# Optimization experiments

Hardware: AMD Instinct MI355X
Metric: run time of the kernel (lower is better)

The kernel has to match this reference:

```python
import jax, jax.numpy as jnp
import numpy as np

B, S, D, H, DH, FF = 4, 4096, 1024, 16, 64, 2048
EPS = 1e-6


def setup_inputs() -> dict:
    key = jax.random.key(0)
    ks = jax.random.split(key, 8)
    s = 0.02
    return {
        "x": jax.random.normal(ks[0], (B, S, D), jnp.float32),
        "scale": jnp.ones((D,), jnp.float32),
        "qw": jax.random.normal(ks[1], (DH * H, D), jnp.float32) * s,
        "qb": jnp.zeros((DH * H,), jnp.float32),
        "kw": jax.random.normal(ks[2], (DH * H, D), jnp.float32) * s,
        "kb": jnp.zeros((DH * H,), jnp.float32),
        "vw": jax.random.normal(ks[3], (DH * H, D), jnp.float32) * s,
        "vb": jnp.zeros((DH * H,), jnp.float32),
        "ow": jax.random.normal(ks[4], (D, DH * H), jnp.float32) * s,
        "ob": jnp.zeros((D,), jnp.float32),
        "f1w": jax.random.normal(ks[5], (FF, D), jnp.float32) * s,
        "f1b": jnp.zeros((FF,), jnp.float32),
        "f2w": jax.random.normal(ks[6], (D, FF), jnp.float32) * s,
        "f2b": jnp.zeros((D,), jnp.float32),
    }


def reference(x, scale, qw, qb, kw, kb, vw, vb, ow, ob, f1w, f1b, f2w, f2b):
    def rms(h):
        return h / jnp.sqrt(jnp.mean(h * h, axis=-1, keepdims=True) + EPS) * scale

    # --- attention (faithful to the module's unusual permutes) ---
    xn = rms(x)
    q = (xn @ qw.T + qb).reshape(B, S, DH, H).transpose(0, 3, 2, 1)  # [B,H,DH,S]
    k = (xn @ kw.T + kb).reshape(B, S, DH, H).transpose(0, 3, 1, 2)  # [B,H,S,DH]
    v = (xn @ vw.T + vb).reshape(B, S, DH, H).transpose(0, 3, 2, 1)  # [B,H,DH,S]
    # scores contract over the SEQUENCE axis -> [B,H,DH,DH]
    att = jax.nn.softmax(jnp.einsum('bhds,bhse->bhde', q, k) / jnp.sqrt(jnp.float32(DH)), axis=-1)
    a = jnp.einsum('bhde,bhes->bhds', att, v)  # [B,H,DH,S]
    # torch: permute(0,2,1,3).reshape(B,-1,DH*H); row-major split of (DH,H,S) -> (S, DH*H)
    a = a.transpose(0, 2, 1, 3).reshape(B, S, DH * H)
    x = a @ ow.T + ob + x

    # --- FFN with the repo's 'SwiGLU' = x*sigmoid(x) + x ---
    xn = rms(x)
    h = xn @ f1w.T + f1b
    h = h * jax.nn.sigmoid(h) + h
    x = h @ f2w.T + f2b + x
    return x
```

## Files before the change

### kernel.cpp

```cpp
#include <hip/hip_runtime.h>
#include <math.h>

typedef unsigned short u16;
typedef __attribute__((ext_vector_type(4))) unsigned short us4;
typedef __attribute__((ext_vector_type(8))) unsigned short us8;
typedef __attribute__((ext_vector_type(4))) float f4;
typedef __attribute__((ext_vector_type(8))) short bf16x8;
typedef __attribute__((ext_vector_type(4))) float f32x4;

#define S_LEN   4096
#define D_MODEL 1024
#define N_HEAD  16
#define D_HEAD  64
#define FF_DIM  2048
#define TOKENS  16384

__device__ __forceinline__ float bf2f(u16 u) {
  union { float f; unsigned u; } x; x.u = ((unsigned)u) << 16; return x.f;
}
__device__ __forceinline__ u16 f2bf(float f) {
  union { float f; unsigned u; } x; x.f = f;
  return (u16)((x.u + 0x7FFFu + ((x.u >> 16) & 1u)) >> 16);
}

__device__ __forceinline__ void gll16(const void* g, void* l) {
  __builtin_amdgcn_global_load_lds(
      (const __attribute__((address_space(1))) void*)g,
      (__attribute__((address_space(3))) void*)l, 16, 0, 0);
}

#define BARF() do { __builtin_amdgcn_s_barrier(); asm volatile("" ::: "memory"); } while (0)

__global__ void __launch_bounds__(256)
cvt6_k(const float* __restrict__ qw, const float* __restrict__ kw,
       const float* __restrict__ vw, const float* __restrict__ ow,
       const float* __restrict__ f1w, const float* __restrict__ f2w,
       u16* __restrict__ wq, u16* __restrict__ wk, u16* __restrict__ wv,
       u16* __restrict__ wo, u16* __restrict__ w1, u16* __restrict__ w2)
{
  const int id = blockIdx.x;
  const float* src; u16* dst; int base;
  if      (id < 1024) { src = qw;  dst = wq; base = 0; }
  else if (id < 2048) { src = kw;  dst = wk; base = 1024; }
  else if (id < 3072) { src = vw;  dst = wv; base = 2048; }
  else if (id < 4096) { src = ow;  dst = wo; base = 3072; }
  else if (id < 6144) { src = f1w; dst = w1; base = 4096; }
  else                { src = f2w; dst = w2; base = 6144; }
  const size_t i = ((size_t)(id - base) * 256 + threadIdx.x) * 4;
  const f4 v = *(const f4*)(src + i);
  us4 o;
  o[0] = f2bf(v[0]); o[1] = f2bf(v[1]); o[2] = f2bf(v[2]); o[3] = f2bf(v[3]);
  *(us4*)(dst + i) = o;
}

__global__ void __launch_bounds__(256)
rmsnorm_k(const float* __restrict__ in, const float* __restrict__ scale,
          u16* __restrict__ out)
{
  const int row = blockIdx.x;
  const int tid = threadIdx.x;
  const f4 v = *(const f4*)(in + (size_t)row * D_MODEL + tid * 4);
  float ss = v[0]*v[0] + v[1]*v[1] + v[2]*v[2] + v[3]*v[3];
#pragma unroll
  for (int off = 32; off > 0; off >>= 1) ss += __shfl_down(ss, off, 64);
  __shared__ float red[4];
  const int wid = tid >> 6, lane = tid & 63;
  if (lane == 0) red[wid] = ss;
  __syncthreads();
  const float tot = red[0] + red[1] + red[2] + red[3];
  const float r = rsqrtf(tot * (1.0f / 1024.0f) + 1e-6f);
  const f4 sc = *(const f4*)(scale + tid * 4);
  us4 o;
  o[0] = f2bf(v[0] * r * sc[0]);
  o[1] = f2bf(v[1] * r * sc[1]);
  o[2] = f2bf(v[2] * r * sc[2]);
  o[3] = f2bf(v[3] * r * sc[3]);
  *(us4*)(out + (size_t)row * D_MODEL + tid * 4) = o;
}

template<int EPI>
__global__ __launch_bounds__(512, 2)
void g8k(const u16* __restrict__ Ag, const u16* __restrict__ Wg,
         const float* __restrict__ bq, const float* __restrict__ bk,
         const float* __restrict__ bv, const float* __restrict__ res,
         void* __restrict__ C0, void* __restrict__ C1, void* __restrict__ C2,
         int N, int K)
{
  __shared__ __align__(16) u16 lds[65536];
  const int tid = threadIdx.x;
  const int w = tid >> 6, l = tid & 63;
  const int fr = l & 15, fq = l >> 4;
  const int wm = w >> 2, wn = w & 3;
  const int m0 = blockIdx.x << 8, n0 = blockIdx.y << 8;
  const int srow = w * 8 + (l >> 3);
  const int scol = ((l & 7) ^ (l >> 3)) << 3;
  const int NT = K >> 6;

  auto STAGE = [&](int isA, int hf, int bfs, int nt) {
    const u16* G = isA ? Ag : Wg;
    const int rb = (isA ? m0 : n0) + hf * 128 + srow;
    const int ks = (nt < NT ? nt << 6 : 0) + scol;
    u16* lb = lds + (isA ? 0 : 32768) + bfs * 16384 + hf * 8192 + w * 512;
    gll16(G + (size_t)rb * K + ks, lb);
    gll16(G + (size_t)(rb + 64) * K + ks, lb + 4096);
  };

  f32x4 acc[8][4] = {};
  bf16x8 afr[4][2], bfr[2][2];

  auto LDA = [&](int bf, int mh) {
#pragma unroll
    for (int i = 0; i < 4; ++i)
#pragma unroll
      for (int kk = 0; kk < 2; ++kk)
        afr[i][kk] = *(const bf16x8*)(lds + bf * 16384 + mh * 8192
                                      + (i * 32 + wm * 16 + fr) * 64
                                      + ((kk * 32 + fq * 8) ^ ((fr & 7) << 3)));
  };
  auto LDB = [&](int bf, int nh) {
#pragma unroll
    for (int jn = 0; jn < 2; ++jn)
#pragma unroll
      for (int kk = 0; kk < 2; ++kk)
        bfr[jn][kk] = *(const bf16x8*)(lds + 32768 + bf * 16384 + nh * 8192
                                       + (jn * 64 + wn * 16 + fr) * 64
                                       + ((kk * 32 + fq * 8) ^ ((fr & 7) << 3)));
  };
  auto MM = [&](int mhalf, int nhalf) {
    __builtin_amdgcn_s_setprio(1);
#pragma unroll
    for (int i = 0; i < 4; ++i)
#pragma unroll
      for (int jn = 0; jn < 2; ++jn)
#pragma unroll
        for (int kk = 0; kk < 2; ++kk)
          acc[mhalf * 4 + i][nhalf * 2 + jn] =
              __builtin_amdgcn_mfma_f32_16x16x32_bf16(afr[i][kk], bfr[jn][kk],
                                                      acc[mhalf * 4 + i][nhalf * 2 + jn], 0, 0, 0);
    __builtin_amdgcn_s_setprio(0);
  };

  STAGE(1, 0, 0, 0);
  STAGE(0, 0, 0, 0);
  STAGE(0, 1, 0, 0);
  STAGE(1, 1, 0, 0);
  STAGE(1, 0, 1, 1);
  STAGE(1, 1, 1, 1);
  asm volatile("s_waitcnt vmcnt(4)" ::: "memory");
  BARF();

  const int NIT = K >> 7;
  for (int it = 0; it < NIT; ++it) {
#pragma unroll
    for (int hf2 = 0; hf2 < 2; ++hf2) {
      const int n = 2 * it + hf2;
      const int bf = n & 1;
      LDA(bf, 0); LDB(bf, 0);
      STAGE(0, 0, bf ^ 1, n + 1);
      BARF();
      MM(0, 0);
      BARF();
      LDB(bf, 1);
      STAGE(0, 1, bf ^ 1, n + 1);
      BARF();
      MM(0, 1);
      BARF();
      LDA(bf, 1);
      STAGE(1, 0, bf, n + 2);
      BARF();
      MM(1, 1);
      BARF();
      LDB(bf, 0);
      STAGE(1, 1, bf, n + 2);
      BARF();
      MM(1, 0);
      asm volatile("s_waitcnt vmcnt(4)" ::: "memory");
      BARF();
    }
  }
  asm volatile("s_waitcnt vmcnt(0)" ::: "memory");
  __builtin_amdgcn_s_barrier();
  asm volatile("" ::: "memory");

  if constexpr (EPI == 2) {
    float* C = (float*)C0;
#pragma unroll
    for (int mi = 0; mi < 8; ++mi)
#pragma unroll
      for (int ni = 0; ni < 4; ++ni) {
        const int c = n0 + ni * 64 + wn * 16 + fr;
        const int r0 = m0 + mi * 32 + wm * 16 + fq * 4;
        const float bb = bq[c];
#pragma unroll
        for (int j = 0; j < 4; ++j)
          C[(size_t)(r0 + j) * N + c] = acc[mi][ni][j] + bb + res[(size_t)(r0 + j) * N + c];
      }
  } else if constexpr (EPI == 3) {
    u16* C = (u16*)C0;
#pragma unroll
    for (int mi = 0; mi < 8; ++mi)
#pragma unroll
      for (int ni = 0; ni < 4; ++ni) {
        const int c = n0 + ni * 64 + wn * 16 + fr;
        const int r0 = m0 + mi * 32 + wm * 16 + fq * 4;
        const float bb = bq[c];
#pragma unroll
        for (int j = 0; j < 4; ++j) {
          const float v = acc[mi][ni][j] + bb;
          const float sig = 1.0f / (1.0f + expf(-v));
          C[(size_t)(r0 + j) * N + c] = f2bf(v * sig + v);
        }
      }
  } else {
    const int z = blockIdx.y >> 2;
    const float* bias = z == 0 ? bq : (z == 1 ? bk : bv);
    const int n0l = n0 & 1023;
    const int bb = m0 >> 12, s0l = m0 & (S_LEN - 1);
#pragma unroll
    for (int mi = 0; mi < 8; ++mi)
#pragma unroll
      for (int ni = 0; ni < 4; ++ni) {
        const int c = ni * 64 + wn * 16 + fr;
        const int r0 = mi * 32 + wm * 16 + fq * 4;
        const float bv_ = bias[n0l + c];
        us4 pk;
#pragma unroll
        for (int j = 0; j < 4; ++j) pk[j] = f2bf(acc[mi][ni][j] + bv_);
        const int byte = ((c << 9) + (r0 << 1)) ^ ((c & 7) << 4);
        *(us4*)((char*)lds + byte) = pk;
      }
    __syncthreads();
    if (z < 2) {
      u16* Cout = z == 0 ? (u16*)C0 : (u16*)C1;
      const int c = tid & 255, half = tid >> 8;
      const int o = n0l + c, d = o >> 4, h = o & 15;
      const int xr = (c & 7) << 4;
      u16* dst = Cout + ((size_t)((bb << 10) + (h << 6) + d)) * S_LEN + s0l + half * 128;
#pragma unroll
      for (int u = 0; u < 16; ++u) {
        const int byte = ((c << 9) + (half << 8) + (u << 4)) ^ xr;
        const us8 v = *(const us8*)((char*)lds + byte);
        *(us8*)(dst + u * 8) = v;
      }
    } else {
      u16* Cv = (u16*)C2;
      const int d0 = n0l >> 4;
#pragma unroll
      for (int q2 = 0; q2 < 8; ++q2) {
        const int idx = q2 * 512 + tid;
        const int h = idx >> 8, r = idx & 255;
        const int xr = (h & 7) << 4;
        us8 lo, hi;
#pragma unroll
        for (int dl = 0; dl < 8; ++dl) {
          lo[dl] = *(const u16*)((char*)lds + ((((h + dl * 16) << 9) + (r << 1)) ^ xr));
          hi[dl] = *(const u16*)((char*)lds + ((((h + (dl + 8) * 16) << 9) + (r << 1)) ^ xr));
        }
        u16* dst = Cv + ((size_t)(bb * 16 + h) * S_LEN + s0l + r) * 64 + d0;
        *(us8*)dst = lo;
        *(us8*)(dst + 8) = hi;
      }
    }
  }
}

__global__ void __launch_bounds__(256)
att_sm_k(const u16* __restrict__ qt, const u16* __restrict__ kt,
         u16* __restrict__ P)
{
  __shared__ float red[4][64][64];
  const int bh = blockIdx.x;
  const int tid = threadIdx.x, w = tid >> 6, l = tid & 63;
  const int fr = l & 15, fq = l >> 4;
  const u16* Qb = qt + (size_t)bh * D_HEAD * S_LEN;
  const u16* Kb = kt + (size_t)bh * D_HEAD * S_LEN;
  f32x4 acc[4][4] = {};
  const int sb = w * 1024 + fq * 8;
  for (int ks = 0; ks < 32; ++ks) {
    const int s0 = sb + ks * 32;
    bf16x8 a[4], b[4];
#pragma unroll
    for (int m = 0; m < 4; ++m)
      a[m] = *(const bf16x8*)(Qb + (size_t)(m*16 + fr) * S_LEN + s0);
#pragma unroll
    for (int n = 0; n < 4; ++n)
      b[n] = *(const bf16x8*)(Kb + (size_t)(n*16 + fr) * S_LEN + s0);
#pragma unroll
    for (int m = 0; m < 4; ++m)
#pragma unroll
      for (int n = 0; n < 4; ++n)
        acc[m][n] = __builtin_amdgcn_mfma_f32_16x16x32_bf16(a[m], b[n], acc[m][n], 0, 0, 0);
  }
#pragma unroll
  for (int m = 0; m < 4; ++m)
#pragma unroll
    for (int n = 0; n < 4; ++n)
      *(f32x4*)&red[w][n*16 + fr][m*16 + fq*4] = acc[m][n];
  __syncthreads();

  const int d = tid >> 2, sub = tid & 3;
  float p[16];
  float mx = -1e30f;
#pragma unroll
  for (int i = 0; i < 16; ++i) {
    const int e = sub * 16 + i;
    float v = red[0][e][d] + red[1][e][d] + red[2][e][d] + red[3][e][d];
    v *= 0.125f;
    p[i] = v; mx = fmaxf(mx, v);
  }
  mx = fmaxf(mx, __shfl_xor(mx, 1, 64));
  mx = fmaxf(mx, __shfl_xor(mx, 2, 64));
  float sm = 0.0f;
#pragma unroll
  for (int i = 0; i < 16; ++i) { p[i] = expf(p[i] - mx); sm += p[i]; }
  sm += __shfl_xor(sm, 1, 64);
  sm += __shfl_xor(sm, 2, 64);
  const float inv = 1.0f / sm;
  us8 o0, o1;
#pragma unroll
  for (int i = 0; i < 8; ++i) { o0[i] = f2bf(p[i] * inv); o1[i] = f2bf(p[i+8] * inv); }
  u16* dst = P + (size_t)bh * 4096 + d * 64 + sub * 16;
  *(us8*)dst = o0;
  *(us8*)(dst + 8) = o1;
}

__global__ void __launch_bounds__(256)
pv2_k(const u16* __restrict__ P, const u16* __restrict__ v2,
      u16* __restrict__ ar)
{
  const int bh = blockIdx.x, sc = blockIdx.y;
  const int b = bh >> 4, h = bh & 15;
  const int tid = threadIdx.x, w = tid >> 6, l = tid & 63;
  const int fr = l & 15, fq = l >> 4;
  const u16* Pb = P + (size_t)bh * 4096;
  const u16* Vb = v2 + (size_t)bh * D_HEAD * S_LEN;

  bf16x8 a[4][2];
#pragma unroll
  for (int m = 0; m < 4; ++m)
#pragma unroll
    for (int ks = 0; ks < 2; ++ks)
      a[m][ks] = *(const bf16x8*)(Pb + (m*16 + fr) * 64 + ks*32 + fq*8);

  const int sw = sc * 512 + w * 128;
  f32x4 acc[8][4] = {};
#pragma unroll
  for (int n = 0; n < 8; ++n) {
    const u16* vp = Vb + (size_t)(sw + n*16 + fr) * 64 + fq*8;
    const bf16x8 b0 = *(const bf16x8*)(vp);
    const bf16x8 b1 = *(const bf16x8*)(vp + 32);
#pragma unroll
    for (int m = 0; m < 4; ++m)
      acc[n][m] = __builtin_amdgcn_mfma_f32_16x16x32_bf16(a[m][0], b0, acc[n][m], 0, 0, 0);
#pragma unroll
    for (int m = 0; m < 4; ++m)
      acc[n][m] = __builtin_amdgcn_mfma_f32_16x16x32_bf16(a[m][1], b1, acc[n][m], 0, 0, 0);
  }

  const int shi = sc >> 1;
  const int col0 = (sc & 1) * 512 + w * 128;
#pragma unroll
  for (int m = 0; m < 4; ++m)
#pragma unroll
    for (int j = 0; j < 4; ++j) {
      const int d = m*16 + fq*4 + j;
      const size_t base = ((size_t)b * 4096 + (d << 6) + (h << 2) + shi) * 1024 + col0;
#pragma unroll
      for (int n = 0; n < 8; ++n)
        ar[base + n*16 + fr] = f2bf(acc[n][m][j]);
    }
}

extern "C" void kernel_launch(void* const* d_in, const int* in_sizes, int n_in,
                              void* d_out, int out_size, void* d_ws, size_t ws_size,
                              hipStream_t stream)
{
  const float* x     = (const float*)d_in[0];
  const float* scale = (const float*)d_in[1];
  const float* qw = (const float*)d_in[2];
  const float* qb = (const float*)d_in[3];
  const float* kw = (const float*)d_in[4];
  const float* kb = (const float*)d_in[5];
  const float* vw = (const float*)d_in[6];
  const float* vb = (const float*)d_in[7];
  const float* ow = (const float*)d_in[8];
  const float* ob = (const float*)d_in[9];
  const float* f1w = (const float*)d_in[10];
  const float* f1b = (const float*)d_in[11];
  const float* f2w = (const float*)d_in[12];
  const float* f2b = (const float*)d_in[13];
  float* out = (float*)d_out;

  const size_t TOKD = (size_t)TOKENS * D_MODEL;
  const size_t WSZ1 = (size_t)D_MODEL * D_MODEL;
  const size_t WSZ2 = (size_t)FF_DIM * D_MODEL;
  u16* xn = (u16*)d_ws;
  u16* qt = xn + TOKD;
  u16* kt = qt + TOKD;
  u16* v2 = kt + TOKD;
  u16* wq = v2 + TOKD;
  u16* wk = wq + WSZ1;
  u16* wv = wk + WSZ1;
  u16* wo = wv + WSZ1;
  u16* w1 = wo + WSZ1;
  u16* w2 = w1 + WSZ2;
  u16* Patt = w2 + WSZ2;
  u16* hbuf = kt;
  u16* ar = qt;

  dim3 blk(256);
  dim3 blk8(512);

  cvt6_k<<<8192, blk, 0, stream>>>(qw, kw, vw, ow, f1w, f2w, wq, wk, wv, wo, w1, w2);
  rmsnorm_k<<<TOKENS, blk, 0, stream>>>(x, scale, xn);
  g8k<0><<<dim3(TOKENS / 256, 12), blk8, 0, stream>>>(
      xn, wq, qb, kb, vb, nullptr, qt, kt, v2, 3072, D_MODEL);
  att_sm_k<<<64, blk, 0, stream>>>(qt, kt, Patt);
  pv2_k<<<dim3(64, 8), blk, 0, stream>>>(Patt, v2, ar);
  g8k<2><<<dim3(TOKENS / 256, D_MODEL / 256), blk8, 0, stream>>>(
      ar, wo, ob, nullptr, nullptr, x, out, nullptr, nullptr, D_MODEL, D_MODEL);
  rmsnorm_k<<<TOKENS, blk, 0, stream>>>(out, scale, xn);
  g8k<3><<<dim3(TOKENS / 256, FF_DIM / 256), blk8, 0, stream>>>(
      xn, w1, f1b, nullptr, nullptr, nullptr, hbuf, nullptr, nullptr, FF_DIM, D_MODEL);
  g8k<2><<<dim3(TOKENS / 256, D_MODEL / 256), blk8, 0, stream>>>(
      hbuf, w2, f2b, nullptr, nullptr, out, out, nullptr, nullptr, D_MODEL, FF_DIM);
}
```

Before: 432.9 us.

## Restructure GEMM main loop: load all B fragments once, stream A per chunk

Replaces the 8-phase ping-pong GEMM loop, which had many barriers per K-tile, with a simpler double-buffered loop. B fragments for all four N-subtiles are loaded once per K-tile, and A fragments are loaded per 16-row chunk just before their MFMAs. This cuts barriers to two per K-tile and changes the prefetch order so that A and B for the next tile go into the alternate buffer. It raises register pressure for B fragments and may expose LDS latency more, since A loads now sit directly in front of their MFMAs.

Result: slower. 442.1 us (+2.1%).

```diff
diff --git a/kernel.cpp b/kernel.cpp
--- a/kernel.cpp
+++ b/kernel.cpp
@@ -106,77 +106,54 @@
   };
 
   f32x4 acc[8][4] = {};
-  bf16x8 afr[4][2], bfr[2][2];
-
-  auto LDA = [&](int bf, int mh) {
-#pragma unroll
-    for (int i = 0; i < 4; ++i)
+  bf16x8 b_frag[4][2];
+
+  auto LDB_ALL = [&](int bf) {
+#pragma unroll
+    for (int ni = 0; ni < 4; ++ni)
 #pragma unroll
       for (int kk = 0; kk < 2; ++kk)
-        afr[i][kk] = *(const bf16x8*)(lds + bf * 16384 + mh * 8192
-                                      + (i * 32 + wm * 16 + fr) * 64
-                                      + ((kk * 32 + fq * 8) ^ ((fr & 7) << 3)));
+        b_frag[ni][kk] = *(const bf16x8*)(lds + 32768 + bf * 16384 + (ni >> 1) * 8192
+                                          + ((ni & 1) * 64 + wn * 16 + fr) * 64
+                                          + ((kk * 32 + fq * 8) ^ ((fr & 7) << 3)));
   };
-  auto LDB = [&](int bf, int nh) {
-#pragma unroll
-    for (int jn = 0; jn < 2; ++jn)
-#pragma unroll
-      for (int kk = 0; kk < 2; ++kk)
-        bfr[jn][kk] = *(const bf16x8*)(lds + 32768 + bf * 16384 + nh * 8192
-                                       + (jn * 64 + wn * 16 + fr) * 64
-                                       + ((kk * 32 + fq * 8) ^ ((fr & 7) << 3)));
-  };
-  auto MM = [&](int mhalf, int nhalf) {
+
+  auto CHUNK = [&](int bf, int mh, int mi) {
+    const u16* base = lds + bf * 16384 + mh * 8192 + (mi * 32 + wm * 16 + fr) * 64;
+    const bf16x8 a0 = *(const bf16x8*)(base + ((fq * 8) ^ ((fr & 7) << 3)));
+    const bf16x8 a1 = *(const bf16x8*)(base + ((32 + fq * 8) ^ ((fr & 7) << 3)));
     __builtin_amdgcn_s_setprio(1);
 #pragma unroll
-    for (int i = 0; i < 4; ++i)
-#pragma unroll
-      for (int jn = 0; jn < 2; ++jn)
-#pragma unroll
-        for (int kk = 0; kk < 2; ++kk)
-          acc[mhalf * 4 + i][nhalf * 2 + jn] =
-              __builtin_amdgcn_mfma_f32_16x16x32_bf16(afr[i][kk], bfr[jn][kk],
-                                                      acc[mhalf * 4 + i][nhalf * 2 + jn], 0, 0, 0);
+    for (int ni = 0; ni < 4; ++ni) {
+      acc[mh * 4 + mi][ni] =
+          __builtin_amdgcn_mfma_f32_16x16x32_bf16(a0, b_frag[ni][0], acc[mh * 4 + mi][ni], 0, 0, 0);
+      acc[mh * 4 + mi][ni] =
+          __builtin_amdgcn_mfma_f32_16x16x32_bf16(a1, b_frag[ni][1], acc[mh * 4 + mi][ni], 0, 0, 0);
+    }
     __builtin_amdgcn_s_setprio(0);
   };
 
-  STAGE(1, 0, 0, 0);
   STAGE(0, 0, 0, 0);
   STAGE(0, 1, 0, 0);
+  STAGE(1, 0, 0, 0);
   STAGE(1, 1, 0, 0);
-  STAGE(1, 0, 1, 1);
-  STAGE(1, 1, 1, 1);
-  asm volatile("s_waitcnt vmcnt(4)" ::: "memory");
+  asm volatile("s_waitcnt vmcnt(2)" ::: "memory");
   BARF();
 
-  const int NIT = K >> 7;
-  for (int it = 0; it < NIT; ++it) {
-#pragma unroll
-    for (int hf2 = 0; hf2 < 2; ++hf2) {
-      const int n = 2 * it + hf2;
-      const int bf = n & 1;
-      LDA(bf, 0); LDB(bf, 0);
-      STAGE(0, 0, bf ^ 1, n + 1);
-      BARF();
-      MM(0, 0);
-      BARF();
-      LDB(bf, 1);
-      STAGE(0, 1, bf ^ 1, n + 1);
-      BARF();
-      MM(0, 1);
-      BARF();
-      LDA(bf, 1);
-      STAGE(1, 0, bf, n + 2);
-      BARF();
-      MM(1, 1);
-      BARF();
-      LDB(bf, 0);
-      STAGE(1, 1, bf, n + 2);
-      BARF();
-      MM(1, 0);
-      asm volatile("s_waitcnt vmcnt(4)" ::: "memory");
-      BARF();
-    }
+#pragma unroll 2
+  for (int t = 0; t < NT; ++t) {
+    const int bf = t & 1;
+    LDB_ALL(bf);
+    STAGE(0, 0, bf ^ 1, t + 1);
+    STAGE(0, 1, bf ^ 1, t + 1);
+    CHUNK(bf, 0, 0); CHUNK(bf, 0, 1); CHUNK(bf, 0, 2); CHUNK(bf, 0, 3);
+    asm volatile("s_waitcnt vmcnt(4)" ::: "memory");
+    BARF();
+    STAGE(1, 0, bf ^ 1, t + 1);
+    STAGE(1, 1, bf ^ 1, t + 1);
+    CHUNK(bf, 1, 0); CHUNK(bf, 1, 1); CHUNK(bf, 1, 2); CHUNK(bf, 1, 3);
+    asm volatile("s_waitcnt vmcnt(2)" ::: "memory");
+    BARF();
   }
   asm volatile("s_waitcnt vmcnt(0)" ::: "memory");
   __builtin_amdgcn_s_barrier();
```

## Fold RMSNorm scale into weights and row norm into GEMM epilogues

Applied to the files above, without the earlier changes.

The RMSNorm scale vector is multiplied into the QKV and FFN1 weights during bf16 conversion, and the per-row inverse RMS is applied in the GEMM epilogue instead of to the activations. The second RMSNorm kernel is removed. The output-projection GEMM now also writes a bf16 copy of the residual output and accumulates per-row sum of squares with atomics, which the FFN1 epilogue turns into the inverse RMS. This drops a full read/write pass over the activations, in exchange for atomics, an extra memset and slightly different rounding because the unnormalized activations are quantized to bf16.

After: 441.4 us. Within noise of the previous version (+2.0%).

```diff
diff --git a/kernel.cpp b/kernel.cpp
--- a/kernel.cpp
+++ b/kernel.cpp
@@ -35,27 +35,31 @@
 cvt6_k(const float* __restrict__ qw, const float* __restrict__ kw,
        const float* __restrict__ vw, const float* __restrict__ ow,
        const float* __restrict__ f1w, const float* __restrict__ f2w,
+       const float* __restrict__ scale,
        u16* __restrict__ wq, u16* __restrict__ wk, u16* __restrict__ wv,
        u16* __restrict__ wo, u16* __restrict__ w1, u16* __restrict__ w2)
 {
   const int id = blockIdx.x;
-  const float* src; u16* dst; int base;
-  if      (id < 1024) { src = qw;  dst = wq; base = 0; }
-  else if (id < 2048) { src = kw;  dst = wk; base = 1024; }
-  else if (id < 3072) { src = vw;  dst = wv; base = 2048; }
-  else if (id < 4096) { src = ow;  dst = wo; base = 3072; }
-  else if (id < 6144) { src = f1w; dst = w1; base = 4096; }
-  else                { src = f2w; dst = w2; base = 6144; }
+  const float* src; u16* dst; int base; bool fold;
+  if      (id < 1024) { src = qw;  dst = wq; base = 0;    fold = true;  }
+  else if (id < 2048) { src = kw;  dst = wk; base = 1024; fold = true;  }
+  else if (id < 3072) { src = vw;  dst = wv; base = 2048; fold = true;  }
+  else if (id < 4096) { src = ow;  dst = wo; base = 3072; fold = false; }
+  else if (id < 6144) { src = f1w; dst = w1; base = 4096; fold = true;  }
+  else                { src = f2w; dst = w2; base = 6144; fold = false; }
   const size_t i = ((size_t)(id - base) * 256 + threadIdx.x) * 4;
   const f4 v = *(const f4*)(src + i);
+  f4 sc = {1.f, 1.f, 1.f, 1.f};
+  if (fold) sc = *(const f4*)(scale + (i & 1023));
   us4 o;
-  o[0] = f2bf(v[0]); o[1] = f2bf(v[1]); o[2] = f2bf(v[2]); o[3] = f2bf(v[3]);
+  o[0] = f2bf(v[0] * sc[0]); o[1] = f2bf(v[1] * sc[1]);
+  o[2] = f2bf(v[2] * sc[2]); o[3] = f2bf(v[3] * sc[3]);
   *(us4*)(dst + i) = o;
 }
 
 __global__ void __launch_bounds__(256)
-rmsnorm_k(const float* __restrict__ in, const float* __restrict__ scale,
-          u16* __restrict__ out)
+cvtx_k(const float* __restrict__ in, u16* __restrict__ xb,
+       float* __restrict__ invr)
 {
   const int row = blockIdx.x;
   const int tid = threadIdx.x;
@@ -67,15 +71,13 @@
   const int wid = tid >> 6, lane = tid & 63;
   if (lane == 0) red[wid] = ss;
   __syncthreads();
-  const float tot = red[0] + red[1] + red[2] + red[3];
-  const float r = rsqrtf(tot * (1.0f / 1024.0f) + 1e-6f);
-  const f4 sc = *(const f4*)(scale + tid * 4);
+  if (tid == 0) {
+    const float tot = red[0] + red[1] + red[2] + red[3];
+    invr[row] = rsqrtf(tot * (1.0f / 1024.0f) + 1e-6f);
+  }
   us4 o;
-  o[0] = f2bf(v[0] * r * sc[0]);
-  o[1] = f2bf(v[1] * r * sc[1]);
-  o[2] = f2bf(v[2] * r * sc[2]);
-  o[3] = f2bf(v[3] * r * sc[3]);
-  *(us4*)(out + (size_t)row * D_MODEL + tid * 4) = o;
+  o[0] = f2bf(v[0]); o[1] = f2bf(v[1]); o[2] = f2bf(v[2]); o[3] = f2bf(v[3]);
+  *(us4*)(xb + (size_t)row * D_MODEL + tid * 4) = o;
 }
 
 template<int EPI>
@@ -195,25 +197,66 @@
         for (int j = 0; j < 4; ++j)
           C[(size_t)(r0 + j) * N + c] = acc[mi][ni][j] + bb + res[(size_t)(r0 + j) * N + c];
       }
+  } else if constexpr (EPI == 4) {
+    float* C = (float*)C0;
+    u16* OB = (u16*)C1;
+    float* SQ = (float*)C2;
+#pragma unroll
+    for (int mi = 0; mi < 8; ++mi) {
+      const int r0 = m0 + mi * 32 + wm * 16 + fq * 4;
+      float part0 = 0.f, part1 = 0.f, part2 = 0.f, part3 = 0.f;
+#pragma unroll
+      for (int ni = 0; ni < 4; ++ni) {
+        const int c = n0 + ni * 64 + wn * 16 + fr;
+        const float bb = bq[c];
+#pragma unroll
+        for (int j = 0; j < 4; ++j) {
+          const float v = acc[mi][ni][j] + bb + res[(size_t)(r0 + j) * N + c];
+          C[(size_t)(r0 + j) * N + c] = v;
+          OB[(size_t)(r0 + j) * N + c] = f2bf(v);
+          if (j == 0) part0 += v * v;
+          else if (j == 1) part1 += v * v;
+          else if (j == 2) part2 += v * v;
+          else part3 += v * v;
+        }
+      }
+      float part[4] = {part0, part1, part2, part3};
+#pragma unroll
+      for (int j = 0; j < 4; ++j) {
+        float p = part[j];
+        p += __shfl_xor(p, 1, 64);
+        p += __shfl_xor(p, 2, 64);
+        p += __shfl_xor(p, 4, 64);
+        p += __shfl_xor(p, 8, 64);
+        if (fr == 0) atomicAdd(&SQ[r0 + j], p);
+      }
+    }
   } else if constexpr (EPI == 3) {
     u16* C = (u16*)C0;
-#pragma unroll
-    for (int mi = 0; mi < 8; ++mi)
+    const float* SQ = res;
+#pragma unroll
+    for (int mi = 0; mi < 8; ++mi) {
+      const int r0 = m0 + mi * 32 + wm * 16 + fq * 4;
+      const f4 sq4 = *(const f4*)(SQ + r0);
+      float iv[4];
+#pragma unroll
+      for (int j = 0; j < 4; ++j) iv[j] = rsqrtf(sq4[j] * (1.0f / 1024.0f) + 1e-6f);
 #pragma unroll
       for (int ni = 0; ni < 4; ++ni) {
         const int c = n0 + ni * 64 + wn * 16 + fr;
-        const int r0 = m0 + mi * 32 + wm * 16 + fq * 4;
         const float bb = bq[c];
 #pragma unroll
         for (int j = 0; j < 4; ++j) {
-          const float v = acc[mi][ni][j] + bb;
+          const float v = acc[mi][ni][j] * iv[j] + bb;
           const float sig = 1.0f / (1.0f + expf(-v));
           C[(size_t)(r0 + j) * N + c] = f2bf(v * sig + v);
         }
       }
+    }
   } else {
     const int z = blockIdx.y >> 2;
     const float* bias = z == 0 ? bq : (z == 1 ? bk : bv);
+    const float* IV = res;
     const int n0l = n0 & 1023;
     const int bb = m0 >> 12, s0l = m0 & (S_LEN - 1);
 #pragma unroll
@@ -222,10 +265,11 @@
       for (int ni = 0; ni < 4; ++ni) {
         const int c = ni * 64 + wn * 16 + fr;
         const int r0 = mi * 32 + wm * 16 + fq * 4;
+        const f4 iv4 = *(const f4*)(IV + m0 + r0);
         const float bv_ = bias[n0l + c];
         us4 pk;
 #pragma unroll
-        for (int j = 0; j < 4; ++j) pk[j] = f2bf(acc[mi][ni][j] + bv_);
+        for (int j = 0; j < 4; ++j) pk[j] = f2bf(acc[mi][ni][j] * iv4[j] + bv_);
         const int byte = ((c << 9) + (r0 << 1)) ^ ((c & 7) << 4);
         *(us4*)((char*)lds + byte) = pk;
       }
@@ -394,8 +438,8 @@
   const size_t TOKD = (size_t)TOKENS * D_MODEL;
   const size_t WSZ1 = (size_t)D_MODEL * D_MODEL;
   const size_t WSZ2 = (size_t)FF_DIM * D_MODEL;
-  u16* xn = (u16*)d_ws;
-  u16* qt = xn + TOKD;
+  u16* xb = (u16*)d_ws;
+  u16* qt = xb + TOKD;
   u16* kt = qt + TOKD;
   u16* v2 = kt + TOKD;
   u16* wq = v2 + TOKD;
@@ -405,23 +449,27 @@
   u16* w1 = wo + WSZ1;
   u16* w2 = w1 + WSZ2;
   u16* Patt = w2 + WSZ2;
+  float* invr1 = (float*)(Patt + (size_t)64 * 64 * 64);
+  float* sumsq = invr1 + TOKENS;
   u16* hbuf = kt;
   u16* ar = qt;
+  u16* outb = xb;
 
   dim3 blk(256);
   dim3 blk8(512);
 
-  cvt6_k<<<8192, blk, 0, stream>>>(qw, kw, vw, ow, f1w, f2w, wq, wk, wv, wo, w1, w2);
-  rmsnorm_k<<<TOKENS, blk, 0, stream>>>(x, scale, xn);
+  hipMemsetAsync(sumsq, 0, TOKENS * sizeof(float), stream);
+  cvt6_k<<<8192, blk, 0, stream>>>(qw, kw, vw, ow, f1w, f2w, scale,
+                                   wq, wk, wv, wo, w1, w2);
+  cvtx_k<<<TOKENS, blk, 0, stream>>>(x, xb, invr1);
   g8k<0><<<dim3(TOKENS / 256, 12), blk8, 0, stream>>>(
-      xn, wq, qb, kb, vb, nullptr, qt, kt, v2, 3072, D_MODEL);
+      xb, wq, qb, kb, vb, invr1, qt, kt, v2, 3072, D_MODEL);
   att_sm_k<<<64, blk, 0, stream>>>(qt, kt, Patt);
   pv2_k<<<dim3(64, 8), blk, 0, stream>>>(Patt, v2, ar);
-  g8k<2><<<dim3(TOKENS / 256, D_MODEL / 256), blk8, 0, stream>>>(
-      ar, wo, ob, nullptr, nullptr, x, out, nullptr, nullptr, D_MODEL, D_MODEL);
-  rmsnorm_k<<<TOKENS, blk, 0, stream>>>(out, scale, xn);
+  g8k<4><<<dim3(TOKENS / 256, D_MODEL / 256), blk8, 0, stream>>>(
+      ar, wo, ob, nullptr, nullptr, x, out, outb, sumsq, D_MODEL, D_MODEL);
   g8k<3><<<dim3(TOKENS / 256, FF_DIM / 256), blk8, 0, stream>>>(
-      xn, w1, f1b, nullptr, nullptr, nullptr, hbuf, nullptr, nullptr, FF_DIM, D_MODEL);
+      outb, w1, f1b, nullptr, nullptr, sumsq, hbuf, nullptr, nullptr, FF_DIM, D_MODEL);
   g8k<2><<<dim3(TOKENS / 256, D_MODEL / 256), blk8, 0, stream>>>(
       hbuf, w2, f2b, nullptr, nullptr, out, out, nullptr, nullptr, D_MODEL, FF_DIM);
 }
```
